# Optimization experiments

Measured on AMD Instinct MI355X. Metric: run time of the kernel, lower is better.

## Reference

```python
import jax, jax.numpy as jnp
import numpy as np

N, E, L, F, M = 512, 2048, 16, 16, 8
HOPS = 2      # egonet radius (k_hop_subgraph num_hops)
H = 128       # WL hash buckets
N_ITER = 3    # WeisfeilerLehman(n_iter=3)
TAU = 0.1     # soft-relabeling temperature


def setup_inputs():
    key = jax.random.key(0)
    k0, k1, k2, k3, k4, k5 = jax.random.split(key, 6)
    labels = jax.random.randint(k0, (N,), 0, L)
    x = jax.nn.one_hot(labels, L, dtype=jnp.float32)
    edge_index = jax.random.randint(k1, (2, E), 0, N)
    # filter adjacencies, built exactly as in GKernel.__init__:
    # symmetric 0/1 with zero diagonal
    A = jax.random.uniform(k2, (F, M, M))
    A = ((A + jnp.swapaxes(A, -1, -2)) > 1.0).astype(jnp.float32)
    A = A * (1.0 - jnp.eye(M, dtype=jnp.float32))
    Xlab = jax.random.randint(k3, (F, M), 0, L)
    X = jax.nn.one_hot(Xlab, L, dtype=jnp.float32)
    # injective label -> bucket embedding (random distinct buckets)
    E0 = jax.nn.one_hot(jax.random.permutation(k4, H)[:L], H, dtype=jnp.float32)
    # random projection used to hash (own-label, neighbor-multiset) signatures
    Rproj = jax.random.normal(k5, (2 * H, H), dtype=jnp.float32)
    return {"x": x, "edge_index": edge_index, "P": A, "X": X, "E0": E0, "Rproj": Rproj}


def _wl_features(c0, nbr_sum, mask, Rproj):
    # soft Weisfeiler-Lehman subtree features: at each iteration the new
    # node label is a hash of (own label, neighbor-label multiset); the
    # graph feature is the concatenated per-iteration label histograms.
    c = c0 * mask[:, None]                       # [n, H]
    feats = [c.sum(0)]
    for _ in range(N_ITER):
        sig = jnp.concatenate([c, nbr_sum(c)], axis=-1)        # [n, 2H]
        c = jax.nn.softmax((sig @ Rproj) / TAU, axis=-1) * mask[:, None]
        feats.append(c.sum(0))
    return jnp.concatenate(feats)                # [(N_ITER+1)*H]


def _max_comp_mask(A):
    # largest connected component via min-label propagation (max_comp)
    comp = jnp.arange(M, dtype=jnp.float32)
    Ab = A > 0
    for _ in range(M):
        nbr_min = jnp.min(jnp.where(Ab, comp[None, :], 1e9), axis=1)
        comp = jnp.minimum(comp, nbr_min)
    ci = comp.astype(jnp.int32)
    counts = jax.ops.segment_sum(jnp.ones(M, jnp.float32), ci, num_segments=M)
    best = jnp.argmax(counts)
    return (ci == best).astype(jnp.float32)


def reference(x, edge_index, P, X, E0, Rproj):
    # symmetrize edges (egonets / WL kernels are undirected)
    src = jnp.concatenate([edge_index[0], edge_index[1]])
    dst = jnp.concatenate([edge_index[1], edge_index[0]])
    # --- k-hop egonet node masks (compute_egonets) : reach[i, j] = 1 iff
    # node j is within HOPS hops of root i ---
    reach = jnp.eye(N, dtype=jnp.float32)
    for _ in range(HOPS):
        agg = jax.ops.segment_sum(reach[:, src].T, dst, num_segments=N).T
        reach = jnp.clip(reach + agg, 0.0, 1.0)
    c0 = x @ E0                                  # initial bucket labels [N, H]

    def ego_feat(mask):
        emask = (mask[src] * mask[dst])[:, None]
        def nbr(c):
            return jax.ops.segment_sum(c[src] * emask, dst, num_segments=N)
        return _wl_features(c0, nbr, mask, Rproj)

    ego_feats = jax.vmap(ego_feat)(reach)        # [N, (N_ITER+1)*H]

    def filt_feat(Af, Xf):
        mask = _max_comp_mask(Af)
        Am = Af * mask[:, None] * mask[None, :]
        return _wl_features(Xf @ E0, lambda c: Am @ c, mask, Rproj)

    filt_feats = jax.vmap(filt_feat)(P, X)       # [F, (N_ITER+1)*H]

    # normalized WL kernel: k(g1,g2)/sqrt(k(g1,g1) k(g2,g2)); sim.T -> [N, F]
    sim = filt_feats @ ego_feats.T               # [F, N]
    nf = jnp.linalg.norm(filt_feats, axis=-1)
    ng = jnp.linalg.norm(ego_feats, axis=-1)
    sim = sim / (nf[:, None] * ng[None, :] + 1e-12)
    return sim.T
```

## Files before the change

kernel.cpp:

```cpp
#include <hip/hip_runtime.h>
#include <hip/hip_bf16.h>

#define NN 512
#define EE 2048
#define LL 16
#define FF 16
#define MM 8
#define HH 128
#define CAP_ROWS 40960
#define MAXD 32
#define TAU_SCALE 14.426950408889634f

typedef __attribute__((ext_vector_type(8))) short bf16x8;
typedef __attribute__((ext_vector_type(4))) float f32x4;

constexpr size_t OFF_ADJ   = 0;
constexpr size_t SZ_ADJ    = (size_t)NN * 8 * 8;
constexpr size_t OFF_DEG   = OFF_ADJ + SZ_ADJ;
constexpr size_t SZ_DEG    = (size_t)NN * 4;
constexpr size_t OFF_CNT   = OFF_DEG + SZ_DEG;
constexpr size_t SZ_CNT    = (size_t)NN * 4;
constexpr size_t OFF_ROFF  = OFF_CNT + SZ_CNT;
constexpr size_t SZ_ROFF   = (size_t)(NN + 1) * 4 + 12;
constexpr size_t OFF_BUCKN = OFF_ROFF + SZ_ROFF;
constexpr size_t SZ_BUCKN  = (size_t)NN * 4;
constexpr size_t OFF_BUCKF = OFF_BUCKN + SZ_BUCKN;
constexpr size_t SZ_BUCKF  = (size_t)FF * MM * 4;
constexpr size_t OFF_NLST  = ((OFF_BUCKF + SZ_BUCKF + 63) / 64) * 64;
constexpr size_t SZ_NLST   = (size_t)NN * MAXD * 2;
constexpr size_t OFF_CEGO  = OFF_NLST + SZ_NLST;
constexpr size_t SZ_CEGO   = (size_t)CAP_ROWS * 2;
constexpr size_t OFF_NCNT  = OFF_CEGO + SZ_CEGO;
constexpr size_t SZ_NCNT   = (size_t)CAP_ROWS * 2;
constexpr size_t OFF_RBK   = OFF_NCNT + SZ_NCNT;
constexpr size_t SZ_RBK    = (size_t)CAP_ROWS * 2;
constexpr size_t OFF_NBR   = OFF_RBK + SZ_RBK;
constexpr size_t SZ_NBR    = (size_t)CAP_ROWS * MAXD * 2;
constexpr size_t OFF_NBK   = OFF_NBR + SZ_NBR;
constexpr size_t SZ_NBK    = (size_t)CAP_ROWS * MAXD * 2;
constexpr size_t OFF_EGOF  = ((OFF_NBK + SZ_NBK + 63) / 64) * 64;
constexpr size_t SZ_EGOF   = (size_t)NN * 512 * 4;
constexpr size_t OFF_FILTF = OFF_EGOF + SZ_EGOF;
constexpr size_t SZ_FILTF  = (size_t)FF * 512 * 4;
constexpr size_t OFF_FNORM = OFF_FILTF + SZ_FILTF;
constexpr size_t SZ_FNORM  = 64;
constexpr size_t OFF_CA    = ((OFF_FNORM + SZ_FNORM + 255) / 256) * 256;
constexpr size_t SZ_CBUF   = (size_t)CAP_ROWS * HH * 4;
constexpr size_t OFF_CB    = OFF_CA + SZ_CBUF;

__device__ __forceinline__ unsigned f2bfbits(float x) {
    unsigned u = __float_as_uint(x);
    return (u + 0x7fffu + ((u >> 16) & 1u)) >> 16;
}
__device__ __forceinline__ float bf2f(unsigned hb) { return __uint_as_float(hb << 16); }

__global__ __launch_bounds__(256) void k_build(const int* __restrict__ ei,
                                               const float* __restrict__ x,
                                               const float* __restrict__ X,
                                               const float* __restrict__ E0,
                                               int* __restrict__ degN,
                                               unsigned short* __restrict__ nbrLstN,
                                               unsigned long long* __restrict__ adj,
                                               int* __restrict__ buckN,
                                               int* __restrict__ buckF) {
    int idx = blockIdx.x * blockDim.x + threadIdx.x;
    if (idx < EE) {
        int a = ei[idx], b = ei[EE + idx];
        int p = atomicAdd(&degN[a], 1);
        if (p < MAXD) nbrLstN[(size_t)a * MAXD + p] = (unsigned short)b;
        int q = atomicAdd(&degN[b], 1);
        if (q < MAXD) nbrLstN[(size_t)b * MAXD + q] = (unsigned short)a;
        atomicOr(&adj[(size_t)a * 8 + (b >> 6)], 1ull << (b & 63));
        atomicOr(&adj[(size_t)b * 8 + (a >> 6)], 1ull << (a & 63));
    } else if (idx < EE + NN) {
        int i = idx - EE;
        int lab = 0;
        for (int l = 0; l < LL; ++l) if (x[i * LL + l] > 0.5f) lab = l;
        int b = 0;
        for (int h = 0; h < HH; ++h) if (E0[lab * HH + h] > 0.5f) b = h;
        buckN[i] = b;
    } else if (idx < EE + NN + FF * MM) {
        int fm = idx - EE - NN;
        int lab = 0;
        for (int l = 0; l < LL; ++l) if (X[fm * LL + l] > 0.5f) lab = l;
        int b = 0;
        for (int h = 0; h < HH; ++h) if (E0[lab * HH + h] > 0.5f) b = h;
        buckF[fm] = b;
    }
}

__global__ __launch_bounds__(64) void k_reach(const unsigned long long* __restrict__ adj,
                                              unsigned long long* __restrict__ bitsR,
                                              int* __restrict__ count) {
    __shared__ unsigned long long r1[8];
    __shared__ unsigned long long r2[8];
    int i = blockIdx.x, t = threadIdx.x;
    if (t < 8) {
        unsigned long long v = adj[(size_t)i * 8 + t];
        if (t == (i >> 6)) v |= 1ull << (i & 63);
        r1[t] = v;
        r2[t] = v;
    }
    __syncthreads();
    unsigned long long p[8] = {0, 0, 0, 0, 0, 0, 0, 0};
    for (int rep = 0; rep < 8; ++rep) {
        if ((r1[rep] >> t) & 1ull) {
            int j = t + rep * 64;
#pragma unroll
            for (int w = 0; w < 8; ++w) p[w] |= adj[(size_t)j * 8 + w];
        }
    }
#pragma unroll
    for (int w = 0; w < 8; ++w)
        if (p[w]) atomicOr(&r2[w], p[w]);
    __syncthreads();
    if (t < 8) bitsR[(size_t)i * 8 + t] = r2[t];
    if (t == 0) {
        int acc = 0;
        for (int w = 0; w < 8; ++w) acc += __popcll(r2[w]);
        count[i] = acc;
    }
}

__global__ __launch_bounds__(512) void k_scan(const int* __restrict__ in,
                                              int* __restrict__ out) {
    __shared__ int s[NN];
    int t = threadIdx.x;
    s[t] = in[t];
    __syncthreads();
    for (int d = 1; d < NN; d <<= 1) {
        int v = (t >= d) ? s[t - d] : 0;
        __syncthreads();
        s[t] += v;
        __syncthreads();
    }
    out[t + 1] = s[t];
    if (t == 0) out[0] = 0;
}

__global__ __launch_bounds__(64) void k_pack(const unsigned long long* __restrict__ bitsR,
                                             const int* __restrict__ count,
                                             const int* __restrict__ rowOff,
                                             const int* __restrict__ degN,
                                             const unsigned short* __restrict__ nbrLstN,
                                             const int* __restrict__ buckN,
                                             unsigned short* __restrict__ nbrRow,
                                             unsigned short* __restrict__ nbrBuck,
                                             unsigned short* __restrict__ nbrCnt,
                                             unsigned short* __restrict__ rowBuck,
                                             unsigned short* __restrict__ cegoG,
                                             float* __restrict__ egoF) {
    __shared__ unsigned long long bits[8];
    __shared__ int wpre[8];
    __shared__ unsigned short cmap_s[NN];
    __shared__ unsigned short nodes_s[NN];
    __shared__ float f0[HH];
    int i = blockIdx.x, t = threadIdx.x;
    if (t < 8) bits[t] = bitsR[(size_t)i * 8 + t];
    if (t < 64) { f0[t] = 0.0f; f0[t + 64] = 0.0f; }
    __syncthreads();
    if (t == 0) {
        int acc = 0;
        for (int w = 0; w < 8; ++w) { wpre[w] = acc; acc += __popcll(bits[w]); }
    }
    __syncthreads();
    int base = rowOff[i];
    int n = count[i];
    if (base >= CAP_ROWS) n = 0;
    else if (base + n > CAP_ROWS) n = CAP_ROWS - base;
    for (int rep = 0; rep < 8; ++rep) {
        int j = t + rep * 64;
        unsigned long long word = bits[rep];
        unsigned short v = 0xFFFFu;
        if ((word >> t) & 1ull) {
            int idx = wpre[rep] + __popcll(word & ((1ull << t) - 1ull));
            if (idx < n) { v = (unsigned short)idx; nodes_s[idx] = (unsigned short)j; }
        }
        cmap_s[j] = v;
    }
    for (int q = 256 + t; q < 512; q += 64) egoF[(size_t)i * 512 + q] = 0.0f;
    __syncthreads();
    for (int m = t; m < n; m += 64) {
        int j = nodes_s[m];
        int b = buckN[j];
        atomicAdd(&f0[b], 1.0f);
        size_t row = (size_t)(base + m);
        rowBuck[row] = (unsigned short)b;
        int dn = degN[j]; if (dn > MAXD) dn = MAXD;
        int cnt = 0;
        for (int e = 0; e < dn; ++e) {
            unsigned short nbNode = nbrLstN[(size_t)j * MAXD + e];
            unsigned short nr = cmap_s[nbNode];
            if (nr != 0xFFFFu && cnt < MAXD) {
                nbrRow[row * MAXD + cnt] = (unsigned short)(base + nr);
                nbrBuck[row * MAXD + cnt] = (unsigned short)buckN[nbNode];
                cnt++;
            }
        }
        nbrCnt[row] = (unsigned short)cnt;
        cegoG[row] = (unsigned short)i;
    }
    __syncthreads();
    if (t < 64) {
        egoF[(size_t)i * 512 + t] = f0[t];
        egoF[(size_t)i * 512 + t + 64] = f0[t + 64];
    }
}

__global__ __launch_bounds__(256) void k_iter1(const int* __restrict__ count,
                                               const int* __restrict__ rowOff,
                                               const unsigned short* __restrict__ rowBuck,
                                               const unsigned short* __restrict__ nbrBuck,
                                               const unsigned short* __restrict__ nbrCnt,
                                               const float* __restrict__ Rg,
                                               float* __restrict__ cOut,
                                               float* __restrict__ egoF) {
    __shared__ float fs[HH];
    int i = blockIdx.x, tid = threadIdx.x;
    int base = rowOff[i];
    int n = count[i];
    if (base >= CAP_ROWS) n = 0;
    else if (base + n > CAP_ROWS) n = CAP_ROWS - base;
    if (tid < HH) fs[tid] = 0.0f;
    __syncthreads();
    const float* Rb = Rg + (size_t)HH * HH;
    int col = (tid & 7) * 16;
    float facc[16];
#pragma unroll
    for (int q = 0; q < 16; ++q) facc[q] = 0.0f;
    for (int m = tid >> 3; m < n; m += 32) {
        int gr = base + m;
        float z[16];
        const float* rt = Rg + (size_t)rowBuck[gr] * HH + col;
#pragma unroll
        for (int q = 0; q < 4; ++q) *(float4*)&z[q * 4] = *(const float4*)&rt[q * 4];
        int cnt = nbrCnt[gr];
        const unsigned short* nk = &nbrBuck[(size_t)gr * MAXD];
        for (int e = 0; e < cnt; ++e) {
            const float* rb = Rb + (size_t)nk[e] * HH + col;
#pragma unroll
            for (int q = 0; q < 4; ++q) {
                float4 rv = *(const float4*)&rb[q * 4];
                z[q * 4 + 0] += rv.x; z[q * 4 + 1] += rv.y;
                z[q * 4 + 2] += rv.z; z[q * 4 + 3] += rv.w;
            }
        }
        float mx = z[0];
#pragma unroll
        for (int q = 1; q < 16; ++q) mx = fmaxf(mx, z[q]);
        for (int off = 4; off > 0; off >>= 1) mx = fmaxf(mx, __shfl_xor(mx, off));
        float s = 0.0f;
#pragma unroll
        for (int q = 0; q < 16; ++q) { z[q] = exp2f((z[q] - mx) * TAU_SCALE); s += z[q]; }
        for (int off = 4; off > 0; off >>= 1) s += __shfl_xor(s, off);
        float inv = 1.0f / s;
        float* crow = cOut + (size_t)gr * HH + col;
#pragma unroll
        for (int q = 0; q < 16; ++q) { z[q] *= inv; facc[q] += z[q]; }
#pragma unroll
        for (int q = 0; q < 4; ++q) *(float4*)&crow[q * 4] = *(const float4*)&z[q * 4];
    }
#pragma unroll
    for (int q = 0; q < 16; ++q) atomicAdd(&fs[col + q], facc[q]);
    __syncthreads();
    if (tid < HH) egoF[(size_t)i * 512 + HH + tid] = fs[tid];
}

__global__ __launch_bounds__(256) void k_prep(const float* __restrict__ Rg,
                                              short* __restrict__ RtH,
                                              short* __restrict__ RtL) {
    int idx = blockIdx.x * blockDim.x + threadIdx.x;
    int col = idx >> 5;
    int kc = (idx & 31) * 8;
    bf16x8 hv, lv;
#pragma unroll
    for (int j = 0; j < 8; ++j) {
        float xv = Rg[(size_t)(kc + j) * HH + col];
        unsigned hb = f2bfbits(xv);
        hv[j] = (short)hb;
        lv[j] = (short)f2bfbits(xv - bf2f(hb));
    }
    *(bf16x8*)&RtH[(size_t)col * 256 + kc] = hv;
    *(bf16x8*)&RtL[(size_t)col * 256 + kc] = lv;
}

__global__ __launch_bounds__(64) void k_iter(const float* __restrict__ cur,
                                             float* __restrict__ nxt,
                                             const short* __restrict__ RtH,
                                             const short* __restrict__ RtL,
                                             const int* __restrict__ rowOff,
                                             const unsigned short* __restrict__ nbrRow,
                                             const unsigned short* __restrict__ nbrCnt,
                                             const unsigned short* __restrict__ cegoG,
                                             float* __restrict__ egoF,
                                             int it) {
    int Rtot = rowOff[NN];
    if (Rtot > CAP_ROWS) Rtot = CAP_ROWS;
    int r0 = blockIdx.x * 16;
    if (r0 >= Rtot) return;
    int tid = threadIdx.x;
    int c16 = tid & 15, g = tid >> 4;
    int kb = g * 8;
    int grA = r0 + c16;
    if (grA >= Rtot) grA = Rtot - 1;

    float ua[4][8];
#pragma unroll
    for (int s = 0; s < 4; ++s)
#pragma unroll
        for (int j = 0; j < 8; ++j) ua[s][j] = 0.0f;
    {
        int cnt = nbrCnt[grA];
        const unsigned short* nb = &nbrRow[(size_t)grA * MAXD];
        for (int e = 0; e < cnt; ++e) {
            const float* cr = &cur[(size_t)nb[e] * HH + kb];
#pragma unroll
            for (int s = 0; s < 4; ++s) {
                float4 v0 = *(const float4*)&cr[s * 32];
                float4 v1 = *(const float4*)&cr[s * 32 + 4];
                ua[s][0] += v0.x; ua[s][1] += v0.y; ua[s][2] += v0.z; ua[s][3] += v0.w;
                ua[s][4] += v1.x; ua[s][5] += v1.y; ua[s][6] += v1.z; ua[s][7] += v1.w;
            }
        }
    }

    f32x4 acc[8];
#pragma unroll
    for (int n = 0; n < 8; ++n) acc[n] = (f32x4)(0.0f);
    const short* bbH = RtH + (size_t)c16 * 256 + kb;
    const short* bbL = RtL + (size_t)c16 * 256 + kb;

#pragma unroll
    for (int s = 0; s < 4; ++s) {
        bf16x8 ahi, alo;
#pragma unroll
        for (int j = 0; j < 8; ++j) {
            float xv = ua[s][j];
            unsigned hb = f2bfbits(xv);
            ahi[j] = (short)hb;
            alo[j] = (short)f2bfbits(xv - bf2f(hb));
        }
        const int t = s + 4;
#pragma unroll
        for (int n = 0; n < 8; ++n) {
            bf16x8 bh = *(const bf16x8*)&bbH[n * 4096 + t * 32];
            bf16x8 bl = *(const bf16x8*)&bbL[n * 4096 + t * 32];
            acc[n] = __builtin_amdgcn_mfma_f32_16x16x32_bf16(ahi, bh, acc[n], 0, 0, 0);
            acc[n] = __builtin_amdgcn_mfma_f32_16x16x32_bf16(ahi, bl, acc[n], 0, 0, 0);
            acc[n] = __builtin_amdgcn_mfma_f32_16x16x32_bf16(alo, bh, acc[n], 0, 0, 0);
        }
    }
    {
        const float* cr = &cur[(size_t)grA * HH + kb];
#pragma unroll
        for (int t = 0; t < 4; ++t) {
            float4 v0 = *(const float4*)&cr[t * 32];
            float4 v1 = *(const float4*)&cr[t * 32 + 4];
            float cv[8] = {v0.x, v0.y, v0.z, v0.w, v1.x, v1.y, v1.z, v1.w};
            bf16x8 ahi, alo;
#pragma unroll
            for (int j = 0; j < 8; ++j) {
                unsigned hb = f2bfbits(cv[j]);
                ahi[j] = (short)hb;
                alo[j] = (short)f2bfbits(cv[j] - bf2f(hb));
            }
#pragma unroll
            for (int n = 0; n < 8; ++n) {
                bf16x8 bh = *(const bf16x8*)&bbH[n * 4096 + t * 32];
                bf16x8 bl = *(const bf16x8*)&bbL[n * 4096 + t * 32];
                acc[n] = __builtin_amdgcn_mfma_f32_16x16x32_bf16(ahi, bh, acc[n], 0, 0, 0);
                acc[n] = __builtin_amdgcn_mfma_f32_16x16x32_bf16(ahi, bl, acc[n], 0, 0, 0);
                acc[n] = __builtin_amdgcn_mfma_f32_16x16x32_bf16(alo, bh, acc[n], 0, 0, 0);
            }
        }
    }

    float inv[4];
#pragma unroll
    for (int i = 0; i < 4; ++i) {
        float m = acc[0][i];
#pragma unroll
        for (int n = 1; n < 8; ++n) m = fmaxf(m, acc[n][i]);
        for (int off = 8; off > 0; off >>= 1) m = fmaxf(m, __shfl_xor(m, off));
        float s = 0.0f;
#pragma unroll
        for (int n = 0; n < 8; ++n) {
            float e = exp2f((acc[n][i] - m) * TAU_SCALE);
            acc[n][i] = e; s += e;
        }
        for (int off = 8; off > 0; off >>= 1) s += __shfl_xor(s, off);
        inv[i] = 1.0f / s;
    }

    float fa[8];
#pragma unroll
    for (int n = 0; n < 8; ++n) fa[n] = 0.0f;
    int cege = -1;
#pragma unroll
    for (int i = 0; i < 4; ++i) {
        int gr = r0 + g * 4 + i;
        if (gr < Rtot) {
#pragma unroll
            for (int n = 0; n < 8; ++n) {
                float c = acc[n][i] * inv[i];
                nxt[(size_t)gr * HH + n * 16 + c16] = c;
                acc[n][i] = c;
            }
            int ego = cegoG[gr];
            if (ego != cege) {
                if (cege >= 0) {
#pragma unroll
                    for (int n = 0; n < 8; ++n) {
                        atomicAdd(&egoF[(size_t)cege * 512 + it * HH + n * 16 + c16], fa[n]);
                        fa[n] = 0.0f;
                    }
                }
                cege = ego;
            }
#pragma unroll
            for (int n = 0; n < 8; ++n) fa[n] += acc[n][i];
        }
    }
    if (cege >= 0) {
#pragma unroll
        for (int n = 0; n < 8; ++n)
            atomicAdd(&egoF[(size_t)cege * 512 + it * HH + n * 16 + c16], fa[n]);
    }
}

__global__ __launch_bounds__(256) void k_filt(const float* __restrict__ P,
                                              const int* __restrict__ buckF,
                                              const float* __restrict__ Rg,
                                              float* __restrict__ filtF,
                                              float* __restrict__ fnorm) {
    __shared__ float As[MM][MM];
    __shared__ float Am[MM][MM];
    __shared__ float msk[MM];
    __shared__ float cbuf[2][MM][HH];
    __shared__ float ubuf[MM][HH];
    __shared__ float feats[4 * HH];
    __shared__ float red4[4];
    int f = blockIdx.x, tid = threadIdx.x, wave = tid >> 6, lane = tid & 63;
    if (tid < 64) As[tid >> 3][tid & 7] = P[f * 64 + tid];
    for (int idx = tid; idx < 4 * HH; idx += 256) feats[idx] = 0.f;
    __syncthreads();
    if (tid == 0) {
        float comp[MM];
        for (int m = 0; m < MM; ++m) comp[m] = (float)m;
        for (int it = 0; it < MM; ++it) {
            float nm[MM];
            for (int j = 0; j < MM; ++j) {
                float mn = 1e9f;
                for (int k = 0; k < MM; ++k)
                    if (As[j][k] > 0.f) mn = fminf(mn, comp[k]);
                nm[j] = mn;
            }
            for (int j = 0; j < MM; ++j) comp[j] = fminf(comp[j], nm[j]);
        }
        int cnt[MM], ci[MM];
        for (int m = 0; m < MM; ++m) cnt[m] = 0;
        for (int m = 0; m < MM; ++m) { ci[m] = (int)comp[m]; cnt[ci[m]]++; }
        int best = 0;
        for (int m = 1; m < MM; ++m) if (cnt[m] > cnt[best]) best = m;
        for (int m = 0; m < MM; ++m) msk[m] = (ci[m] == best) ? 1.0f : 0.0f;
    }
    __syncthreads();
    if (tid < 64) Am[tid >> 3][tid & 7] = As[tid >> 3][tid & 7] * msk[tid >> 3] * msk[tid & 7];
    for (int idx = tid; idx < MM * HH; idx += 256) {
        int m = idx >> 7, h = idx & 127;
        cbuf[0][m][h] = (msk[m] > 0.f && h == buckF[f * MM + m]) ? 1.0f : 0.0f;
    }
    __syncthreads();
    if (tid < HH) {
        float s = 0.f;
        for (int m = 0; m < MM; ++m) s += cbuf[0][m][tid];
        feats[tid] = s;
    }
    __syncthreads();
    int cur = 0;
    int h2 = 2 * lane;
    for (int it = 1; it <= 3; ++it) {
#pragma unroll
        for (int jj = 0; jj < 2; ++jj) {
            int d = wave * 2 + jj;
            float u0 = 0.f, u1 = 0.f;
            for (int s = 0; s < MM; ++s) {
                float w = Am[d][s];
                u0 += w * cbuf[cur][s][h2];
                u1 += w * cbuf[cur][s][h2 + 1];
            }
            ubuf[d][h2] = u0;
            ubuf[d][h2 + 1] = u1;
        }
        float a0[2] = {0.f, 0.f}, a1[2] = {0.f, 0.f};
        for (int k = 0; k < HH; ++k) {
            float2 rt = *(const float2*)&Rg[(size_t)k * HH + h2];
            float2 rb = *(const float2*)&Rg[(size_t)(HH + k) * HH + h2];
#pragma unroll
            for (int jj = 0; jj < 2; ++jj) {
                int d = wave * 2 + jj;
                float cd = cbuf[cur][d][k];
                float ud = ubuf[d][k];
                a0[jj] += cd * rt.x + ud * rb.x;
                a1[jj] += cd * rt.y + ud * rb.y;
            }
        }
#pragma unroll
        for (int jj = 0; jj < 2; ++jj) {
            int d = wave * 2 + jj;
            float z0 = a0[jj], z1 = a1[jj];
            float m = fmaxf(z0, z1);
            for (int off = 32; off > 0; off >>= 1) m = fmaxf(m, __shfl_xor(m, off));
            float e0 = exp2f((z0 - m) * TAU_SCALE);
            float e1 = exp2f((z1 - m) * TAU_SCALE);
            float s = e0 + e1;
            for (int off = 32; off > 0; off >>= 1) s += __shfl_xor(s, off);
            float inv = msk[d] / s;
            float c0 = e0 * inv, c1 = e1 * inv;
            cbuf[1 - cur][d][h2] = c0;
            cbuf[1 - cur][d][h2 + 1] = c1;
            atomicAdd(&feats[it * HH + h2], c0);
            atomicAdd(&feats[it * HH + h2 + 1], c1);
        }
        __syncthreads();
        cur = 1 - cur;
    }
    float np = 0.f;
    for (int idx = tid; idx < 4 * HH; idx += 256) {
        float v = feats[idx];
        filtF[(size_t)f * 512 + idx] = v;
        np += v * v;
    }
    for (int off = 32; off > 0; off >>= 1) np += __shfl_xor(np, off);
    if (lane == 0) red4[wave] = np;
    __syncthreads();
    if (tid == 0) fnorm[f] = sqrtf(red4[0] + red4[1] + red4[2] + red4[3]);
}

__global__ __launch_bounds__(64) void k_sim(const float* __restrict__ egoF,
                                            const float* __restrict__ filtF,
                                            const float* __restrict__ fnorm,
                                            float* __restrict__ out) {
    int i = blockIdx.x, lane = threadIdx.x;
    float e[8];
    float ss = 0.f;
#pragma unroll
    for (int r = 0; r < 8; ++r) {
        e[r] = egoF[(size_t)i * 512 + r * 64 + lane];
        ss += e[r] * e[r];
    }
    for (int off = 32; off > 0; off >>= 1) ss += __shfl_xor(ss, off);
    float ng = sqrtf(ss);
    for (int f = 0; f < FF; ++f) {
        float d = 0.f;
#pragma unroll
        for (int r = 0; r < 8; ++r) d += e[r] * filtF[(size_t)f * 512 + r * 64 + lane];
        for (int off = 32; off > 0; off >>= 1) d += __shfl_xor(d, off);
        if (lane == 0) out[i * FF + f] = d / (fnorm[f] * ng + 1e-12f);
    }
}

extern "C" void kernel_launch(void* const* d_in, const int* in_sizes, int n_in,
                              void* d_out, int out_size, void* d_ws, size_t ws_size,
                              hipStream_t stream) {
    (void)in_sizes; (void)n_in; (void)out_size; (void)ws_size;
    const float* x  = (const float*)d_in[0];
    const int*   ei = (const int*)d_in[1];
    const float* P  = (const float*)d_in[2];
    const float* X  = (const float*)d_in[3];
    const float* E0 = (const float*)d_in[4];
    const float* Rg = (const float*)d_in[5];
    float* out = (float*)d_out;
    char* ws = (char*)d_ws;

    unsigned long long* adj   = (unsigned long long*)(ws + OFF_ADJ);
    int* degN   = (int*)(ws + OFF_DEG);
    int* count  = (int*)(ws + OFF_CNT);
    int* rowOff = (int*)(ws + OFF_ROFF);
    int* buckN  = (int*)(ws + OFF_BUCKN);
    int* buckF  = (int*)(ws + OFF_BUCKF);
    unsigned short* nbrLstN = (unsigned short*)(ws + OFF_NLST);
    unsigned short* cego    = (unsigned short*)(ws + OFF_CEGO);
    unsigned short* nbrCnt  = (unsigned short*)(ws + OFF_NCNT);
    unsigned short* rowBuck = (unsigned short*)(ws + OFF_RBK);
    unsigned short* nbrRow  = (unsigned short*)(ws + OFF_NBR);
    unsigned short* nbrBuck = (unsigned short*)(ws + OFF_NBK);
    float* egoF  = (float*)(ws + OFF_EGOF);
    float* filtF = (float*)(ws + OFF_FILTF);
    float* fnorm = (float*)(ws + OFF_FNORM);
    float* cA    = (float*)(ws + OFF_CA);
    float* cB    = (float*)(ws + OFF_CB);
    unsigned long long* bitsR = (unsigned long long*)(ws + OFF_CA);
    short* RtH = (short*)(ws + OFF_NBK);
    short* RtL = RtH + (size_t)HH * 256;

    hipMemsetAsync(ws, 0, OFF_CNT, stream);
    k_build<<<(EE + NN + FF * MM + 255) / 256, 256, 0, stream>>>(ei, x, X, E0, degN, nbrLstN,
                                                                 adj, buckN, buckF);
    k_reach<<<NN, 64, 0, stream>>>(adj, bitsR, count);
    k_scan<<<1, 512, 0, stream>>>(count, rowOff);
    k_pack<<<NN, 64, 0, stream>>>(bitsR, count, rowOff, degN, nbrLstN, buckN,
                                  nbrRow, nbrBuck, nbrCnt, rowBuck, cego, egoF);
    k_iter1<<<NN, 256, 0, stream>>>(count, rowOff, rowBuck, nbrBuck, nbrCnt, Rg, cB, egoF);
    k_prep<<<16, 256, 0, stream>>>(Rg, RtH, RtL);
    k_iter<<<CAP_ROWS / 16, 64, 0, stream>>>(cB, cA, RtH, RtL, rowOff, nbrRow, nbrCnt, cego, egoF, 2);
    k_iter<<<CAP_ROWS / 16, 64, 0, stream>>>(cA, cB, RtH, RtL, rowOff, nbrRow, nbrCnt, cego, egoF, 3);
    k_filt<<<FF, 256, 0, stream>>>(P, buckF, Rg, filtF, fnorm);
    k_sim<<<NN, 64, 0, stream>>>(egoF, filtF, fnorm, out);
}
```

Before: 305.7 us.

## Split k_iter work across two waves per 16-row tile

Each k_iter block now runs two waves. The neighbor-sum gather is split between them by edge halves and combined through shared memory, and the output columns are split so each wave computes 4 of the 8 MFMA column tiles. The softmax max and sum are reduced across the two waves via shared memory with extra barriers. The neighbor loop is also unrolled by two so more loads are in flight. The aim is more parallelism and latency hiding per row tile, at the cost of three __syncthreads, redundant own-row conversion in both waves, and added LDS use.

```diff
diff --git a/kernel.cpp b/kernel.cpp
--- a/kernel.cpp
+++ b/kernel.cpp
@@ -284,7 +284,7 @@
     *(bf16x8*)&RtL[(size_t)col * 256 + kc] = lv;
 }
 
-__global__ __launch_bounds__(64) void k_iter(const float* __restrict__ cur,
+__global__ __launch_bounds__(128, 4) void k_iter(const float* __restrict__ cur,
                                              float* __restrict__ nxt,
                                              const short* __restrict__ RtH,
                                              const short* __restrict__ RtL,
@@ -294,12 +294,17 @@
                                              const unsigned short* __restrict__ cegoG,
                                              float* __restrict__ egoF,
                                              int it) {
+    __shared__ float us[2][16][HH + 4];
+    __shared__ float smax[2][16];
+    __shared__ float ssum[2][16];
     int Rtot = rowOff[NN];
     if (Rtot > CAP_ROWS) Rtot = CAP_ROWS;
     int r0 = blockIdx.x * 16;
     if (r0 >= Rtot) return;
     int tid = threadIdx.x;
-    int c16 = tid & 15, g = tid >> 4;
+    int w = tid >> 6;
+    int lane = tid & 63;
+    int c16 = lane & 15, g = lane >> 4;
     int kb = g * 8;
     int grA = r0 + c16;
     if (grA >= Rtot) grA = Rtot - 1;
@@ -311,24 +316,64 @@
         for (int j = 0; j < 8; ++j) ua[s][j] = 0.0f;
     {
         int cnt = nbrCnt[grA];
+        int half = cnt >> 1;
+        int e0 = w ? half : 0;
+        int e1 = w ? cnt : half;
         const unsigned short* nb = &nbrRow[(size_t)grA * MAXD];
-        for (int e = 0; e < cnt; ++e) {
-            const float* cr = &cur[(size_t)nb[e] * HH + kb];
+        int e = e0;
+        for (; e + 1 < e1; e += 2) {
+            const float* pa = &cur[(size_t)nb[e] * HH + kb];
+            const float* pb = &cur[(size_t)nb[e + 1] * HH + kb];
+            float4 va[8], vb[8];
 #pragma unroll
             for (int s = 0; s < 4; ++s) {
-                float4 v0 = *(const float4*)&cr[s * 32];
-                float4 v1 = *(const float4*)&cr[s * 32 + 4];
+                va[2 * s]     = *(const float4*)&pa[s * 32];
+                va[2 * s + 1] = *(const float4*)&pa[s * 32 + 4];
+                vb[2 * s]     = *(const float4*)&pb[s * 32];
+                vb[2 * s + 1] = *(const float4*)&pb[s * 32 + 4];
+            }
+#pragma unroll
+            for (int s = 0; s < 4; ++s) {
+                ua[s][0] += va[2 * s].x + vb[2 * s].x;
+                ua[s][1] += va[2 * s].y + vb[2 * s].y;
+                ua[s][2] += va[2 * s].z + vb[2 * s].z;
+                ua[s][3] += va[2 * s].w + vb[2 * s].w;
+                ua[s][4] += va[2 * s + 1].x + vb[2 * s + 1].x;
+                ua[s][5] += va[2 * s + 1].y + vb[2 * s + 1].y;
+                ua[s][6] += va[2 * s + 1].z + vb[2 * s + 1].z;
+                ua[s][7] += va[2 * s + 1].w + vb[2 * s + 1].w;
+            }
+        }
+        if (e < e1) {
+            const float* pa = &cur[(size_t)nb[e] * HH + kb];
+#pragma unroll
+            for (int s = 0; s < 4; ++s) {
+                float4 v0 = *(const float4*)&pa[s * 32];
+                float4 v1 = *(const float4*)&pa[s * 32 + 4];
                 ua[s][0] += v0.x; ua[s][1] += v0.y; ua[s][2] += v0.z; ua[s][3] += v0.w;
                 ua[s][4] += v1.x; ua[s][5] += v1.y; ua[s][6] += v1.z; ua[s][7] += v1.w;
             }
         }
     }
-
-    f32x4 acc[8];
-#pragma unroll
-    for (int n = 0; n < 8; ++n) acc[n] = (f32x4)(0.0f);
-    const short* bbH = RtH + (size_t)c16 * 256 + kb;
-    const short* bbL = RtL + (size_t)c16 * 256 + kb;
+#pragma unroll
+    for (int s = 0; s < 4; ++s) {
+        *(float4*)&us[w][c16][s * 32 + kb]     = *(float4*)&ua[s][0];
+        *(float4*)&us[w][c16][s * 32 + kb + 4] = *(float4*)&ua[s][4];
+    }
+    __syncthreads();
+#pragma unroll
+    for (int s = 0; s < 4; ++s) {
+        float4 o0 = *(const float4*)&us[1 - w][c16][s * 32 + kb];
+        float4 o1 = *(const float4*)&us[1 - w][c16][s * 32 + kb + 4];
+        ua[s][0] += o0.x; ua[s][1] += o0.y; ua[s][2] += o0.z; ua[s][3] += o0.w;
+        ua[s][4] += o1.x; ua[s][5] += o1.y; ua[s][6] += o1.z; ua[s][7] += o1.w;
+    }
+
+    f32x4 acc[4];
+#pragma unroll
+    for (int n = 0; n < 4; ++n) acc[n] = (f32x4)(0.0f);
+    const short* bbH = RtH + (size_t)(4 * w + 0) * 4096 + (size_t)c16 * 256 + kb;
+    const short* bbL = RtL + (size_t)(4 * w + 0) * 4096 + (size_t)c16 * 256 + kb;
 
 #pragma unroll
     for (int s = 0; s < 4; ++s) {
@@ -342,7 +387,7 @@
         }
         const int t = s + 4;
 #pragma unroll
-        for (int n = 0; n < 8; ++n) {
+        for (int n = 0; n < 4; ++n) {
             bf16x8 bh = *(const bf16x8*)&bbH[n * 4096 + t * 32];
             bf16x8 bl = *(const bf16x8*)&bbL[n * 4096 + t * 32];
             acc[n] = __builtin_amdgcn_mfma_f32_16x16x32_bf16(ahi, bh, acc[n], 0, 0, 0);
@@ -365,7 +410,7 @@
                 alo[j] = (short)f2bfbits(cv[j] - bf2f(hb));
             }
 #pragma unroll
-            for (int n = 0; n < 8; ++n) {
+            for (int n = 0; n < 4; ++n) {
                 bf16x8 bh = *(const bf16x8*)&bbH[n * 4096 + t * 32];
                 bf16x8 bl = *(const bf16x8*)&bbL[n * 4096 + t * 32];
                 acc[n] = __builtin_amdgcn_mfma_f32_16x16x32_bf16(ahi, bh, acc[n], 0, 0, 0);
@@ -375,56 +420,68 @@
         }
     }
 
-    float inv[4];
+    float lmax[4];
 #pragma unroll
     for (int i = 0; i < 4; ++i) {
         float m = acc[0][i];
 #pragma unroll
-        for (int n = 1; n < 8; ++n) m = fmaxf(m, acc[n][i]);
+        for (int n = 1; n < 4; ++n) m = fmaxf(m, acc[n][i]);
         for (int off = 8; off > 0; off >>= 1) m = fmaxf(m, __shfl_xor(m, off));
+        lmax[i] = m;
+        if (c16 == 0) smax[w][4 * g + i] = m;
+    }
+    __syncthreads();
+    float inv[4];
+#pragma unroll
+    for (int i = 0; i < 4; ++i) {
+        float m = fmaxf(smax[0][4 * g + i], smax[1][4 * g + i]);
         float s = 0.0f;
 #pragma unroll
-        for (int n = 0; n < 8; ++n) {
+        for (int n = 0; n < 4; ++n) {
             float e = exp2f((acc[n][i] - m) * TAU_SCALE);
             acc[n][i] = e; s += e;
         }
         for (int off = 8; off > 0; off >>= 1) s += __shfl_xor(s, off);
-        inv[i] = 1.0f / s;
-    }
-
-    float fa[8];
-#pragma unroll
-    for (int n = 0; n < 8; ++n) fa[n] = 0.0f;
+        if (c16 == 0) ssum[w][4 * g + i] = s;
+    }
+    __syncthreads();
+#pragma unroll
+    for (int i = 0; i < 4; ++i)
+        inv[i] = 1.0f / (ssum[0][4 * g + i] + ssum[1][4 * g + i]);
+
+    float fa[4];
+#pragma unroll
+    for (int n = 0; n < 4; ++n) fa[n] = 0.0f;
     int cege = -1;
 #pragma unroll
     for (int i = 0; i < 4; ++i) {
         int gr = r0 + g * 4 + i;
         if (gr < Rtot) {
 #pragma unroll
-            for (int n = 0; n < 8; ++n) {
+            for (int n = 0; n < 4; ++n) {
                 float c = acc[n][i] * inv[i];
-                nxt[(size_t)gr * HH + n * 16 + c16] = c;
+                nxt[(size_t)gr * HH + (4 * w + n) * 16 + c16] = c;
                 acc[n][i] = c;
             }
             int ego = cegoG[gr];
             if (ego != cege) {
                 if (cege >= 0) {
 #pragma unroll
-                    for (int n = 0; n < 8; ++n) {
-                        atomicAdd(&egoF[(size_t)cege * 512 + it * HH + n * 16 + c16], fa[n]);
+                    for (int n = 0; n < 4; ++n) {
+                        atomicAdd(&egoF[(size_t)cege * 512 + it * HH + (4 * w + n) * 16 + c16], fa[n]);
                         fa[n] = 0.0f;
                     }
                 }
                 cege = ego;
             }
 #pragma unroll
-            for (int n = 0; n < 8; ++n) fa[n] += acc[n][i];
+            for (int n = 0; n < 4; ++n) fa[n] += acc[n][i];
         }
     }
     if (cege >= 0) {
 #pragma unroll
-        for (int n = 0; n < 8; ++n)
-            atomicAdd(&egoF[(size_t)cege * 512 + it * HH + n * 16 + c16], fa[n]);
+        for (int n = 0; n < 4; ++n)
+            atomicAdd(&egoF[(size_t)cege * 512 + it * HH + (4 * w + n) * 16 + c16], fa[n]);
     }
 }
 
@@ -603,8 +660,8 @@
                                   nbrRow, nbrBuck, nbrCnt, rowBuck, cego, egoF);
     k_iter1<<<NN, 256, 0, stream>>>(count, rowOff, rowBuck, nbrBuck, nbrCnt, Rg, cB, egoF);
     k_prep<<<16, 256, 0, stream>>>(Rg, RtH, RtL);
-    k_iter<<<CAP_ROWS / 16, 64, 0, stream>>>(cB, cA, RtH, RtL, rowOff, nbrRow, nbrCnt, cego, egoF, 2);
-    k_iter<<<CAP_ROWS / 16, 64, 0, stream>>>(cA, cB, RtH, RtL, rowOff, nbrRow, nbrCnt, cego, egoF, 3);
+    k_iter<<<CAP_ROWS / 16, 128, 0, stream>>>(cB, cA, RtH, RtL, rowOff, nbrRow, nbrCnt, cego, egoF, 2);
+    k_iter<<<CAP_ROWS / 16, 128, 0, stream>>>(cA, cB, RtH, RtL, rowOff, nbrRow, nbrCnt, cego, egoF, 3);
     k_filt<<<FF, 256, 0, stream>>>(P, buckF, Rg, filtF, fnorm);
     k_sim<<<NN, 64, 0, stream>>>(egoF, filtF, fnorm, out);
 }
```

Result: slower. 320.3 us (+4.8%).

## Restructure k_iter as persistent 4-wave blocks with register-resident weights

Applied to the files above, without the earlier changes.

k_iter becomes a persistent 256-thread kernel. Each wave keeps its 32-column slice of the split-bf16 Rproj in registers for the whole launch instead of reloading it per 16-row tile. Rows are gathered cooperatively: half the threads load the own label and half sum the neighbours. Both halves are converted to hi/lo bf16 and staged in a swizzled LDS tile shared by the four waves. The softmax is then reduced across waves through shared memory, which adds three barriers per tile and much higher register pressure in exchange for removing repeated weight fetches and tiny 64-thread blocks.

```diff
diff --git a/kernel.cpp b/kernel.cpp
--- a/kernel.cpp
+++ b/kernel.cpp
@@ -284,7 +284,7 @@
     *(bf16x8*)&RtL[(size_t)col * 256 + kc] = lv;
 }
 
-__global__ __launch_bounds__(64) void k_iter(const float* __restrict__ cur,
+__global__ __launch_bounds__(256, 2) void k_iter(const float* __restrict__ cur,
                                              float* __restrict__ nxt,
                                              const short* __restrict__ RtH,
                                              const short* __restrict__ RtL,
@@ -294,137 +294,144 @@
                                              const unsigned short* __restrict__ cegoG,
                                              float* __restrict__ egoF,
                                              int it) {
+    __shared__ unsigned short aH[16 * 256];
+    __shared__ unsigned short aL[16 * 256];
+    __shared__ float smax[4][16];
+    __shared__ float ssum[4][16];
     int Rtot = rowOff[NN];
     if (Rtot > CAP_ROWS) Rtot = CAP_ROWS;
-    int r0 = blockIdx.x * 16;
-    if (r0 >= Rtot) return;
     int tid = threadIdx.x;
-    int c16 = tid & 15, g = tid >> 4;
+    int w = tid >> 6, lane = tid & 63;
+    int c16 = lane & 15, g = lane >> 4;
     int kb = g * 8;
-    int grA = r0 + c16;
-    if (grA >= Rtot) grA = Rtot - 1;
-
-    float ua[4][8];
-#pragma unroll
-    for (int s = 0; s < 4; ++s)
-#pragma unroll
-        for (int j = 0; j < 8; ++j) ua[s][j] = 0.0f;
-    {
-        int cnt = nbrCnt[grA];
-        const unsigned short* nb = &nbrRow[(size_t)grA * MAXD];
-        for (int e = 0; e < cnt; ++e) {
-            const float* cr = &cur[(size_t)nb[e] * HH + kb];
-#pragma unroll
-            for (int s = 0; s < 4; ++s) {
-                float4 v0 = *(const float4*)&cr[s * 32];
-                float4 v1 = *(const float4*)&cr[s * 32 + 4];
-                ua[s][0] += v0.x; ua[s][1] += v0.y; ua[s][2] += v0.z; ua[s][3] += v0.w;
-                ua[s][4] += v1.x; ua[s][5] += v1.y; ua[s][6] += v1.z; ua[s][7] += v1.w;
-            }
-        }
-    }
-
-    f32x4 acc[8];
-#pragma unroll
-    for (int n = 0; n < 8; ++n) acc[n] = (f32x4)(0.0f);
-    const short* bbH = RtH + (size_t)c16 * 256 + kb;
-    const short* bbL = RtL + (size_t)c16 * 256 + kb;
-
-#pragma unroll
-    for (int s = 0; s < 4; ++s) {
-        bf16x8 ahi, alo;
-#pragma unroll
-        for (int j = 0; j < 8; ++j) {
-            float xv = ua[s][j];
-            unsigned hb = f2bfbits(xv);
-            ahi[j] = (short)hb;
-            alo[j] = (short)f2bfbits(xv - bf2f(hb));
-        }
-        const int t = s + 4;
-#pragma unroll
-        for (int n = 0; n < 8; ++n) {
-            bf16x8 bh = *(const bf16x8*)&bbH[n * 4096 + t * 32];
-            bf16x8 bl = *(const bf16x8*)&bbL[n * 4096 + t * 32];
-            acc[n] = __builtin_amdgcn_mfma_f32_16x16x32_bf16(ahi, bh, acc[n], 0, 0, 0);
-            acc[n] = __builtin_amdgcn_mfma_f32_16x16x32_bf16(ahi, bl, acc[n], 0, 0, 0);
-            acc[n] = __builtin_amdgcn_mfma_f32_16x16x32_bf16(alo, bh, acc[n], 0, 0, 0);
-        }
-    }
-    {
-        const float* cr = &cur[(size_t)grA * HH + kb];
-#pragma unroll
-        for (int t = 0; t < 4; ++t) {
-            float4 v0 = *(const float4*)&cr[t * 32];
-            float4 v1 = *(const float4*)&cr[t * 32 + 4];
-            float cv[8] = {v0.x, v0.y, v0.z, v0.w, v1.x, v1.y, v1.z, v1.w};
-            bf16x8 ahi, alo;
+    bf16x8 bHreg[2][8], bLreg[2][8];
+#pragma unroll
+    for (int n = 0; n < 2; ++n) {
+        const short* pH = RtH + (size_t)((2 * w + n) * 16 + c16) * 256 + kb;
+        const short* pL = RtL + (size_t)((2 * w + n) * 16 + c16) * 256 + kb;
+#pragma unroll
+        for (int t = 0; t < 8; ++t) {
+            bHreg[n][t] = *(const bf16x8*)&pH[t * 32];
+            bLreg[n][t] = *(const bf16x8*)&pL[t * 32];
+        }
+    }
+    int grow = tid >> 4;
+    int seg = tid & 15;
+    for (int r0 = blockIdx.x * 16; r0 < Rtot; r0 += gridDim.x * 16) {
+        int grG = r0 + grow; if (grG >= Rtot) grG = Rtot - 1;
+        float v[16];
+        if (seg < 8) {
+            const float* cr = &cur[(size_t)grG * HH + seg * 16];
+#pragma unroll
+            for (int q = 0; q < 4; ++q) {
+                float4 t4 = *(const float4*)&cr[q * 4];
+                v[q * 4 + 0] = t4.x; v[q * 4 + 1] = t4.y;
+                v[q * 4 + 2] = t4.z; v[q * 4 + 3] = t4.w;
+            }
+        } else {
+#pragma unroll
+            for (int q = 0; q < 16; ++q) v[q] = 0.0f;
+            int cnt = nbrCnt[grG];
+            const unsigned short* nb = &nbrRow[(size_t)grG * MAXD];
+            int c0 = (seg - 8) * 16;
+            for (int e = 0; e < cnt; ++e) {
+                const float* cr = &cur[(size_t)nb[e] * HH + c0];
+#pragma unroll
+                for (int q = 0; q < 4; ++q) {
+                    float4 t4 = *(const float4*)&cr[q * 4];
+                    v[q * 4 + 0] += t4.x; v[q * 4 + 1] += t4.y;
+                    v[q * 4 + 2] += t4.z; v[q * 4 + 3] += t4.w;
+                }
+            }
+        }
+        {
+            int kc = seg * 16;
+            unsigned sw = (unsigned)((grow & 7) << 4);
+            unsigned byte0 = ((unsigned)(grow * 512 + kc * 2)) ^ sw;
+            unsigned byte1 = ((unsigned)(grow * 512 + kc * 2 + 16)) ^ sw;
+            bf16x8 h0, h1, l0, l1;
 #pragma unroll
             for (int j = 0; j < 8; ++j) {
-                unsigned hb = f2bfbits(cv[j]);
-                ahi[j] = (short)hb;
-                alo[j] = (short)f2bfbits(cv[j] - bf2f(hb));
-            }
-#pragma unroll
-            for (int n = 0; n < 8; ++n) {
-                bf16x8 bh = *(const bf16x8*)&bbH[n * 4096 + t * 32];
-                bf16x8 bl = *(const bf16x8*)&bbL[n * 4096 + t * 32];
-                acc[n] = __builtin_amdgcn_mfma_f32_16x16x32_bf16(ahi, bh, acc[n], 0, 0, 0);
-                acc[n] = __builtin_amdgcn_mfma_f32_16x16x32_bf16(ahi, bl, acc[n], 0, 0, 0);
-                acc[n] = __builtin_amdgcn_mfma_f32_16x16x32_bf16(alo, bh, acc[n], 0, 0, 0);
-            }
-        }
-    }
-
-    float inv[4];
-#pragma unroll
-    for (int i = 0; i < 4; ++i) {
-        float m = acc[0][i];
-#pragma unroll
-        for (int n = 1; n < 8; ++n) m = fmaxf(m, acc[n][i]);
-        for (int off = 8; off > 0; off >>= 1) m = fmaxf(m, __shfl_xor(m, off));
-        float s = 0.0f;
-#pragma unroll
-        for (int n = 0; n < 8; ++n) {
-            float e = exp2f((acc[n][i] - m) * TAU_SCALE);
-            acc[n][i] = e; s += e;
-        }
-        for (int off = 8; off > 0; off >>= 1) s += __shfl_xor(s, off);
-        inv[i] = 1.0f / s;
-    }
-
-    float fa[8];
-#pragma unroll
-    for (int n = 0; n < 8; ++n) fa[n] = 0.0f;
-    int cege = -1;
-#pragma unroll
-    for (int i = 0; i < 4; ++i) {
-        int gr = r0 + g * 4 + i;
-        if (gr < Rtot) {
-#pragma unroll
-            for (int n = 0; n < 8; ++n) {
-                float c = acc[n][i] * inv[i];
-                nxt[(size_t)gr * HH + n * 16 + c16] = c;
-                acc[n][i] = c;
-            }
-            int ego = cegoG[gr];
-            if (ego != cege) {
-                if (cege >= 0) {
-#pragma unroll
-                    for (int n = 0; n < 8; ++n) {
-                        atomicAdd(&egoF[(size_t)cege * 512 + it * HH + n * 16 + c16], fa[n]);
-                        fa[n] = 0.0f;
+                unsigned hb = f2bfbits(v[j]);
+                h0[j] = (short)hb;
+                l0[j] = (short)f2bfbits(v[j] - bf2f(hb));
+                unsigned hb2 = f2bfbits(v[8 + j]);
+                h1[j] = (short)hb2;
+                l1[j] = (short)f2bfbits(v[8 + j] - bf2f(hb2));
+            }
+            *(bf16x8*)((char*)aH + byte0) = h0;
+            *(bf16x8*)((char*)aH + byte1) = h1;
+            *(bf16x8*)((char*)aL + byte0) = l0;
+            *(bf16x8*)((char*)aL + byte1) = l1;
+        }
+        __syncthreads();
+        f32x4 acc0 = (f32x4)(0.0f), acc1 = (f32x4)(0.0f);
+#pragma unroll
+        for (int tt = 0; tt < 8; ++tt) {
+            const int t = (tt < 4) ? tt + 4 : tt - 4;
+            unsigned abyte = ((unsigned)(c16 * 512 + (kb + 32 * t) * 2)) ^ ((unsigned)((c16 & 7) << 4));
+            bf16x8 ah = *(const bf16x8*)((const char*)aH + abyte);
+            bf16x8 al = *(const bf16x8*)((const char*)aL + abyte);
+            acc0 = __builtin_amdgcn_mfma_f32_16x16x32_bf16(ah, bHreg[0][t], acc0, 0, 0, 0);
+            acc0 = __builtin_amdgcn_mfma_f32_16x16x32_bf16(ah, bLreg[0][t], acc0, 0, 0, 0);
+            acc0 = __builtin_amdgcn_mfma_f32_16x16x32_bf16(al, bHreg[0][t], acc0, 0, 0, 0);
+            acc1 = __builtin_amdgcn_mfma_f32_16x16x32_bf16(ah, bHreg[1][t], acc1, 0, 0, 0);
+            acc1 = __builtin_amdgcn_mfma_f32_16x16x32_bf16(ah, bLreg[1][t], acc1, 0, 0, 0);
+            acc1 = __builtin_amdgcn_mfma_f32_16x16x32_bf16(al, bHreg[1][t], acc1, 0, 0, 0);
+        }
+#pragma unroll
+        for (int i = 0; i < 4; ++i) {
+            float m = fmaxf(acc0[i], acc1[i]);
+            for (int off = 8; off > 0; off >>= 1) m = fmaxf(m, __shfl_xor(m, off));
+            if (c16 == 0) smax[w][4 * g + i] = m;
+        }
+        __syncthreads();
+        float inv[4];
+#pragma unroll
+        for (int i = 0; i < 4; ++i) {
+            int rr = 4 * g + i;
+            float m = fmaxf(fmaxf(smax[0][rr], smax[1][rr]), fmaxf(smax[2][rr], smax[3][rr]));
+            float e0 = exp2f((acc0[i] - m) * TAU_SCALE);
+            float e1 = exp2f((acc1[i] - m) * TAU_SCALE);
+            acc0[i] = e0; acc1[i] = e1;
+            float s = e0 + e1;
+            for (int off = 8; off > 0; off >>= 1) s += __shfl_xor(s, off);
+            if (c16 == 0) ssum[w][rr] = s;
+        }
+        __syncthreads();
+#pragma unroll
+        for (int i = 0; i < 4; ++i) {
+            int rr = 4 * g + i;
+            inv[i] = 1.0f / (ssum[0][rr] + ssum[1][rr] + ssum[2][rr] + ssum[3][rr]);
+        }
+        float fa0 = 0.f, fa1 = 0.f;
+        int cege = -1;
+        int col0 = (2 * w + 0) * 16 + c16;
+        int col1 = (2 * w + 1) * 16 + c16;
+#pragma unroll
+        for (int i = 0; i < 4; ++i) {
+            int gr = r0 + g * 4 + i;
+            if (gr < Rtot) {
+                float c0v = acc0[i] * inv[i];
+                float c1v = acc1[i] * inv[i];
+                nxt[(size_t)gr * HH + col0] = c0v;
+                nxt[(size_t)gr * HH + col1] = c1v;
+                int ego = cegoG[gr];
+                if (ego != cege) {
+                    if (cege >= 0) {
+                        atomicAdd(&egoF[(size_t)cege * 512 + it * HH + col0], fa0);
+                        atomicAdd(&egoF[(size_t)cege * 512 + it * HH + col1], fa1);
+                        fa0 = 0.f; fa1 = 0.f;
                     }
+                    cege = ego;
                 }
-                cege = ego;
-            }
-#pragma unroll
-            for (int n = 0; n < 8; ++n) fa[n] += acc[n][i];
-        }
-    }
-    if (cege >= 0) {
-#pragma unroll
-        for (int n = 0; n < 8; ++n)
-            atomicAdd(&egoF[(size_t)cege * 512 + it * HH + n * 16 + c16], fa[n]);
+                fa0 += c0v; fa1 += c1v;
+            }
+        }
+        if (cege >= 0) {
+            atomicAdd(&egoF[(size_t)cege * 512 + it * HH + col0], fa0);
+            atomicAdd(&egoF[(size_t)cege * 512 + it * HH + col1], fa1);
+        }
     }
 }
 
@@ -603,8 +610,8 @@
                                   nbrRow, nbrBuck, nbrCnt, rowBuck, cego, egoF);
     k_iter1<<<NN, 256, 0, stream>>>(count, rowOff, rowBuck, nbrBuck, nbrCnt, Rg, cB, egoF);
     k_prep<<<16, 256, 0, stream>>>(Rg, RtH, RtL);
-    k_iter<<<CAP_ROWS / 16, 64, 0, stream>>>(cB, cA, RtH, RtL, rowOff, nbrRow, nbrCnt, cego, egoF, 2);
-    k_iter<<<CAP_ROWS / 16, 64, 0, stream>>>(cA, cB, RtH, RtL, rowOff, nbrRow, nbrCnt, cego, egoF, 3);
+    k_iter<<<512, 256, 0, stream>>>(cB, cA, RtH, RtL, rowOff, nbrRow, nbrCnt, cego, egoF, 2);
+    k_iter<<<512, 256, 0, stream>>>(cA, cB, RtH, RtL, rowOff, nbrRow, nbrCnt, cego, egoF, 3);
     k_filt<<<FF, 256, 0, stream>>>(P, buckF, Rg, filtF, fnorm);
     k_sim<<<NN, 64, 0, stream>>>(egoF, filtF, fnorm, out);
 }
```

Result: no change. 311.1 us (+1.8%).
